# Kernel optimization log

Measured on AMD Instinct MI355X. Metric: run time of the kernel, lower is better.

Reference implementation:

```python
import jax, jax.numpy as jnp
import numpy as np

H = 8              # n_heads
N_PER_GRAPH = 64   # nodes per graph (equal-sized graphs)


def setup_inputs() -> dict:
    key = jax.random.key(0)
    ks = jax.random.split(key, 5)
    total, D = 65536, 512
    x = jax.random.normal(ks[0], (total, D), dtype=jnp.float32)
    batch = jnp.arange(total, dtype=jnp.int64) // N_PER_GRAPH  # sorted graph ids
    s = 1.0 / np.sqrt(D).astype(np.float32)
    # nn.MultiheadAttention packed in-proj (xavier-ish uniform) + zero bias
    in_proj_w = jax.random.uniform(ks[1], (3 * D, D), jnp.float32, -s, s)
    in_proj_b = jnp.zeros((3 * D,), jnp.float32)
    out_proj_w = jax.random.uniform(ks[2], (D, D), jnp.float32, -s, s)
    out_proj_b = jnp.zeros((D,), jnp.float32)
    gate_w = jax.random.uniform(ks[3], (1, D), jnp.float32, -s, s)
    gate_b = jnp.zeros((1,), jnp.float32)
    return {"x": x, "batch": batch, "in_proj_w": in_proj_w, "in_proj_b": in_proj_b,
            "out_proj_w": out_proj_w, "out_proj_b": out_proj_b,
            "gate_w": gate_w, "gate_b": gate_b}


def reference(x, batch, in_proj_w, in_proj_b, out_proj_w, out_proj_b, gate_w, gate_b):
    total, D = x.shape
    G = total // N_PER_GRAPH
    hd = D // H
    xg = x.reshape(G, N_PER_GRAPH, D)                       # [G, N, D]
    # packed qkv projection (torch: x @ in_proj_w.T + in_proj_b)
    qkv = jnp.einsum('gnd,ed->gne', xg, in_proj_w) + in_proj_b
    q, k, v = jnp.split(qkv, 3, axis=-1)
    def to_heads(t):
        return t.reshape(G, N_PER_GRAPH, H, hd).transpose(0, 2, 1, 3)  # [G, H, N, hd]
    q, k, v = to_heads(q), to_heads(k), to_heads(v)
    scores = jnp.einsum('ghnd,ghmd->ghnm', q, k) * (1.0 / np.sqrt(hd))
    attn = jax.nn.softmax(scores, axis=-1)
    ctx = jnp.einsum('ghnm,ghmd->ghnd', attn, v)
    ctx = ctx.transpose(0, 2, 1, 3).reshape(G, N_PER_GRAPH, D)
    attn_out = jnp.einsum('gnd,ed->gne', ctx, out_proj_w) + out_proj_b  # [G, N, D]
    gates = jax.nn.sigmoid(jnp.einsum('gnd,od->gno', attn_out, gate_w) + gate_b)
    return (attn_out * gates).sum(axis=1)                   # [G, D]
```

## Files before the change

### kernel.cpp

```cpp
#include <hip/hip_runtime.h>
#include <stdint.h>


typedef __attribute__((ext_vector_type(8))) short short8;
typedef __attribute__((ext_vector_type(4))) float f32x4;

#define D_ 512

#define WQKV_OFF   0u
#define WO_OFF     1572864u
#define UPART_OFF  2097152u
#define U_OFF      2129920u
#define C0_OFF     2131968u
#define SG_OFF     2132032u
#define WCTX_OFF   2136128u

__device__ __forceinline__ unsigned short f2bf(float f) {
    union { float f; unsigned int u; } t; t.f = f;
    unsigned int u = t.u;
    return (unsigned short)((u + 0x7FFFu + ((u >> 16) & 1u)) >> 16);
}

__global__ __launch_bounds__(256)
void convert_weights(const float* __restrict__ wqkv, const float* __restrict__ wo,
                     unsigned short* __restrict__ wbf) {
    const int i4 = blockIdx.x * 256 + threadIdx.x;
    float4 v;
    if (i4 < 196608) v = *(const float4*)(wqkv + (size_t)i4 * 4);
    else             v = *(const float4*)(wo   + (size_t)(i4 - 196608) * 4);
    unsigned short a0 = f2bf(v.x), a1 = f2bf(v.y), a2 = f2bf(v.z), a3 = f2bf(v.w);
    uint2 p; p.x = a0 | ((unsigned)a1 << 16); p.y = a2 | ((unsigned)a3 << 16);
    *(uint2*)(wbf + (size_t)i4 * 4) = p;
}

__global__ __launch_bounds__(256)
void compute_u_partial(const float* __restrict__ wo, const float* __restrict__ gw,
                       float* __restrict__ upart) {
    const int b = blockIdx.x;
    const int t = threadIdx.x;
    float a0 = 0.f, a1 = 0.f;
    #pragma unroll 4
    for (int e = b * 32; e < b * 32 + 32; ++e) {
        const float ge = gw[e];
        a0 += wo[(size_t)e * 512 + t]       * ge;
        a1 += wo[(size_t)e * 512 + t + 256] * ge;
    }
    upart[b * 512 + t] = a0; upart[b * 512 + t + 256] = a1;
}

__global__ __launch_bounds__(256)
void finalize_u(const float* __restrict__ upart, const float* __restrict__ bo,
                const float* __restrict__ gw, const float* __restrict__ gb,
                float* __restrict__ u, float* __restrict__ c0) {
    const int t = threadIdx.x;
    float s0 = 0.f, s1 = 0.f;
    #pragma unroll
    for (int b = 0; b < 16; ++b) { s0 += upart[b*512 + t]; s1 += upart[b*512 + t + 256]; }
    u[t] = s0; u[t + 256] = s1;
    __shared__ float rb[256];
    rb[t] = bo[t] * gw[t] + bo[t + 256] * gw[t + 256];
    __syncthreads();
    for (int s = 128; s > 0; s >>= 1) { if (t < s) rb[t] += rb[t + s]; __syncthreads(); }
    if (t == 0) c0[0] = rb[0] + gb[0];
}

__global__ __launch_bounds__(512, 2)
void attn_ctx_kernel(const float* __restrict__ x,
                     const unsigned short* __restrict__ wqkv,
                     const float* __restrict__ bqkv,
                     const float* __restrict__ u,
                     const float* __restrict__ c0,
                     unsigned short* __restrict__ wctx_ws,
                     float* __restrict__ sumgate)
{
    __shared__ unsigned short xs[64][520];
    __shared__ unsigned short qbuf[2][64][72];
    __shared__ unsigned short kbuf[2][64][72];
    __shared__ unsigned short vbuf[2][64][72];
    __shared__ unsigned short pbuf[2][64][72];
    __shared__ float fbuf[4][512];
    __shared__ float logit2[2][64];
    __shared__ float gatev[64];

    const int g    = blockIdx.x;
    const int tid  = threadIdx.x;
    const int w    = tid >> 6;
    const int lane = tid & 63;
    const int l15  = lane & 15;
    const int quad = lane >> 4;

    #pragma unroll
    for (int i = 0; i < 16; ++i) {
        int idx = tid + i * 512;
        int row = idx >> 7;
        int c4  = idx & 127;
        float4 v = *(const float4*)(x + ((size_t)(g*64 + row))*512 + c4*4);
        unsigned short a0 = f2bf(v.x), a1 = f2bf(v.y), a2 = f2bf(v.z), a3 = f2bf(v.w);
        uint2 p; p.x = a0 | ((unsigned)a1 << 16); p.y = a2 | ((unsigned)a3 << 16);
        *(uint2*)(&xs[row][c4*4]) = p;
    }
    if (tid < 128) ((float*)logit2)[tid] = 0.f;

    const int hs2  = w >> 2;
    const int row0 = (w & 3) << 4;
    f32x4 cctx[4][4];

    int mj[3], hsj[3], rtj[3];
    #pragma unroll
    for (int j = 0; j < 3; ++j) {
        int t_ = w*3 + j;
        int c  = t_ >> 2; rtj[j] = t_ & 3;
        mj[j]  = c >> 1;  hsj[j] = c & 1;
    }

    #pragma unroll
    for (int hp = 0; hp < 4; ++hp) {
        __syncthreads();

        f32x4 acc[3][4];
        #pragma unroll
        for (int j = 0; j < 3; ++j)
            #pragma unroll
            for (int nt = 0; nt < 4; ++nt) acc[j][nt] = (f32x4){0.f,0.f,0.f,0.f};

        const unsigned short* wr[3];
        #pragma unroll
        for (int j = 0; j < 3; ++j) {
            int head = hp*2 + hsj[j];
            wr[j] = wqkv + (size_t)(mj[j]*512 + head*64 + rtj[j]*16 + l15) * 512;
        }
        #pragma unroll 4
        for (int ks = 0; ks < 16; ++ks) {
            const int col = ks*32 + quad*8;
            short8 a0 = *(const short8*)(wr[0] + col);
            short8 a1 = *(const short8*)(wr[1] + col);
            short8 a2 = *(const short8*)(wr[2] + col);
            #pragma unroll
            for (int nt = 0; nt < 4; ++nt) {
                short8 b = *(const short8*)(&xs[nt*16 + l15][col]);
                acc[0][nt] = __builtin_amdgcn_mfma_f32_16x16x32_bf16(a0, b, acc[0][nt], 0,0,0);
                acc[1][nt] = __builtin_amdgcn_mfma_f32_16x16x32_bf16(a1, b, acc[1][nt], 0,0,0);
                acc[2][nt] = __builtin_amdgcn_mfma_f32_16x16x32_bf16(a2, b, acc[2][nt], 0,0,0);
            }
        }
        #pragma unroll
        for (int j = 0; j < 3; ++j) {
            const int head  = hp*2 + hsj[j];
            const int dbase = mj[j]*512 + head*64 + rtj[j]*16 + quad*4;
            if (mj[j] == 2) {
                #pragma unroll
                for (int nt = 0; nt < 4; ++nt)
                    #pragma unroll
                    for (int r = 0; r < 4; ++r)
                        vbuf[hsj[j]][rtj[j]*16 + quad*4 + r][nt*16 + l15] =
                            f2bf(acc[j][nt][r] + bqkv[dbase + r]);
            } else {
                unsigned short (*dst)[72] = (mj[j] == 0) ? qbuf[hsj[j]] : kbuf[hsj[j]];
                #pragma unroll
                for (int nt = 0; nt < 4; ++nt) {
                    unsigned short tv[4];
                    #pragma unroll
                    for (int r = 0; r < 4; ++r) tv[r] = f2bf(acc[j][nt][r] + bqkv[dbase + r]);
                    uint2 pk; pk.x = tv[0] | ((unsigned)tv[1] << 16);
                    pk.y = tv[2] | ((unsigned)tv[3] << 16);
                    *(uint2*)(&dst[nt*16 + l15][rtj[j]*16 + quad*4]) = pk;
                }
            }
        }
        __syncthreads();

        f32x4 sacc[4];
        #pragma unroll
        for (int i = 0; i < 4; ++i) sacc[i] = (f32x4){0.f,0.f,0.f,0.f};
        #pragma unroll
        for (int ks = 0; ks < 2; ++ks) {
            short8 aq = *(const short8*)(&qbuf[hs2][row0 + l15][ks*32 + quad*8]);
            #pragma unroll
            for (int mt = 0; mt < 4; ++mt) {
                short8 bk = *(const short8*)(&kbuf[hs2][mt*16 + l15][ks*32 + quad*8]);
                sacc[mt] = __builtin_amdgcn_mfma_f32_16x16x32_bf16(aq, bk, sacc[mt], 0,0,0);
            }
        }
        float pv[4][4];
        #pragma unroll
        for (int r = 0; r < 4; ++r) {
            float m0 = -1e30f;
            #pragma unroll
            for (int mt = 0; mt < 4; ++mt) { pv[mt][r] = sacc[mt][r] * 0.125f; m0 = fmaxf(m0, pv[mt][r]); }
            m0 = fmaxf(m0, __shfl_xor(m0, 1));
            m0 = fmaxf(m0, __shfl_xor(m0, 2));
            m0 = fmaxf(m0, __shfl_xor(m0, 4));
            m0 = fmaxf(m0, __shfl_xor(m0, 8));
            float s = 0.f;
            #pragma unroll
            for (int mt = 0; mt < 4; ++mt) { float e = __expf(pv[mt][r] - m0); pv[mt][r] = e; s += e; }
            s += __shfl_xor(s, 1); s += __shfl_xor(s, 2); s += __shfl_xor(s, 4); s += __shfl_xor(s, 8);
            float inv = 1.0f / s;
            #pragma unroll
            for (int mt = 0; mt < 4; ++mt) pv[mt][r] *= inv;
        }
        #pragma unroll
        for (int mt = 0; mt < 4; ++mt)
            #pragma unroll
            for (int r = 0; r < 4; ++r)
                pbuf[hs2][row0 + quad*4 + r][mt*16 + l15] = f2bf(pv[mt][r]);
        __syncthreads();

        #pragma unroll
        for (int i = 0; i < 4; ++i) cctx[hp][i] = (f32x4){0.f,0.f,0.f,0.f};
        #pragma unroll
        for (int ks = 0; ks < 2; ++ks) {
            short8 ap = *(const short8*)(&pbuf[hs2][row0 + l15][ks*32 + quad*8]);
            #pragma unroll
            for (int dt = 0; dt < 4; ++dt) {
                short8 bv = *(const short8*)(&vbuf[hs2][dt*16 + l15][ks*32 + quad*8]);
                cctx[hp][dt] = __builtin_amdgcn_mfma_f32_16x16x32_bf16(ap, bv, cctx[hp][dt], 0,0,0);
            }
        }
        {
            const int head2 = hp*2 + hs2;
            float uv[4];
            #pragma unroll
            for (int dt = 0; dt < 4; ++dt) uv[dt] = u[head2*64 + dt*16 + l15];
            #pragma unroll
            for (int r = 0; r < 4; ++r) {
                float s = cctx[hp][0][r]*uv[0] + cctx[hp][1][r]*uv[1]
                        + cctx[hp][2][r]*uv[2] + cctx[hp][3][r]*uv[3];
                s += __shfl_xor(s, 1); s += __shfl_xor(s, 2);
                s += __shfl_xor(s, 4); s += __shfl_xor(s, 8);
                if (l15 == 0) logit2[hs2][row0 + quad*4 + r] += s;
            }
        }
    }

    __syncthreads();
    if (tid < 64) {
        float lg = logit2[0][tid] + logit2[1][tid] + c0[0];
        float gt = 1.0f / (1.0f + __expf(-lg));
        gatev[tid] = gt;
        float s = gt;
        s += __shfl_xor(s, 1);  s += __shfl_xor(s, 2);  s += __shfl_xor(s, 4);
        s += __shfl_xor(s, 8);  s += __shfl_xor(s, 16); s += __shfl_xor(s, 32);
        if (tid == 0) sumgate[g] = s;
    }
    __syncthreads();

    {
        float gv[4];
        #pragma unroll
        for (int r = 0; r < 4; ++r) gv[r] = gatev[row0 + quad*4 + r];
        #pragma unroll
        for (int hp = 0; hp < 4; ++hp) {
            const int head2 = hp*2 + hs2;
            #pragma unroll
            for (int dt = 0; dt < 4; ++dt) {
                float s = cctx[hp][dt][0]*gv[0] + cctx[hp][dt][1]*gv[1]
                        + cctx[hp][dt][2]*gv[2] + cctx[hp][dt][3]*gv[3];
                s += __shfl_xor(s, 16); s += __shfl_xor(s, 32);
                if (lane < 16) fbuf[w & 3][head2*64 + dt*16 + lane] = s;
            }
        }
    }
    __syncthreads();
    {
        float vs = fbuf[0][tid] + fbuf[1][tid] + fbuf[2][tid] + fbuf[3][tid];
        wctx_ws[(size_t)g*512 + tid] = f2bf(vs);
    }
}

__global__ __launch_bounds__(256, 4)
void outproj_kernel(const unsigned short* __restrict__ wo_bf,
                    const unsigned short* __restrict__ wctx_bf,
                    const float* __restrict__ bo,
                    const float* __restrict__ sumgate,
                    float* __restrict__ out)
{
    const int tid  = threadIdx.x;
    const int w    = tid >> 6;
    const int lane = tid & 63;
    const int l15  = lane & 15;
    const int quad = lane >> 4;
    const int g0   = blockIdx.x * 32;

    f32x4 oac[8][2];
    #pragma unroll
    for (int et = 0; et < 8; ++et)
        #pragma unroll
        for (int mt = 0; mt < 2; ++mt)
            oac[et][mt] = (f32x4){0.f,0.f,0.f,0.f};

    #pragma unroll 4
    for (int ks = 0; ks < 16; ++ks) {
        const int col = ks*32 + quad*8;
        short8 a0 = *(const short8*)(wctx_bf + (size_t)(g0 + l15)*D_      + col);
        short8 a1 = *(const short8*)(wctx_bf + (size_t)(g0 + 16 + l15)*D_ + col);
        #pragma unroll
        for (int et = 0; et < 8; ++et) {
            short8 b = *(const short8*)(wo_bf + (size_t)(w*128 + et*16 + l15)*D_ + col);
            oac[et][0] = __builtin_amdgcn_mfma_f32_16x16x32_bf16(a0, b, oac[et][0], 0,0,0);
            oac[et][1] = __builtin_amdgcn_mfma_f32_16x16x32_bf16(a1, b, oac[et][1], 0,0,0);
        }
    }
    #pragma unroll
    for (int et = 0; et < 8; ++et) {
        const int e = w*128 + et*16 + l15;
        const float bov = bo[e];
        #pragma unroll
        for (int mt = 0; mt < 2; ++mt)
            #pragma unroll
            for (int r = 0; r < 4; ++r) {
                const int gg = g0 + mt*16 + quad*4 + r;
                out[(size_t)gg*D_ + e] = oac[et][mt][r] + sumgate[gg] * bov;
            }
    }
}

extern "C" void kernel_launch(void* const* d_in, const int* in_sizes, int n_in,
                              void* d_out, int out_size, void* d_ws, size_t ws_size,
                              hipStream_t stream) {
    const float* x    = (const float*)d_in[0];
    const float* wqkv = (const float*)d_in[2];
    const float* bqkv = (const float*)d_in[3];
    const float* wo   = (const float*)d_in[4];
    const float* bo   = (const float*)d_in[5];
    const float* gw   = (const float*)d_in[6];
    const float* gb   = (const float*)d_in[7];
    float* out = (float*)d_out;

    char* ws = (char*)d_ws;
    unsigned short* wqkv_bf = (unsigned short*)(ws + WQKV_OFF);
    unsigned short* wo_bf   = (unsigned short*)(ws + WO_OFF);
    float*          upart   = (float*)(ws + UPART_OFF);
    float*          u_ws    = (float*)(ws + U_OFF);
    float*          c0_ws   = (float*)(ws + C0_OFF);
    float*          sg_ws   = (float*)(ws + SG_OFF);
    unsigned short* wctx_ws = (unsigned short*)(ws + WCTX_OFF);

    const int total = in_sizes[0] / D_;
    const int G     = total / 64;

    hipLaunchKernelGGL(convert_weights,   dim3(1024), dim3(256), 0, stream, wqkv, wo, wqkv_bf);
    hipLaunchKernelGGL(compute_u_partial, dim3(16),   dim3(256), 0, stream, wo, gw, upart);
    hipLaunchKernelGGL(finalize_u,        dim3(1),    dim3(256), 0, stream, upart, bo, gw, gb, u_ws, c0_ws);
    hipLaunchKernelGGL(attn_ctx_kernel,   dim3(G),    dim3(512), 0, stream,
                       x, wqkv_bf, bqkv, u_ws, c0_ws, wctx_ws, sg_ws);
    hipLaunchKernelGGL(outproj_kernel,    dim3(G/32), dim3(256), 0, stream,
                       wo_bf, wctx_ws, bo, sg_ws, out);
}
```

Before: 477.5 us.

## Assign one head per wave and keep Q/K in registers to drop block barriers

Each of the 8 waves now owns one attention head end to end: it computes Q, K and V for that head, rearranges Q and K into MFMA operand layout in registers with lane shuffles, and runs scores, softmax and P·V inside the wave. A private per-wave shared-memory scratch holds only V and P. This removes the four head-pair iterations and their repeated __syncthreads. The gated context reduction is also written directly from registers, dropping the fbuf stage. In exchange, register pressure rises (16 score tiles and 16 context tiles per wave), which could cause spills at the 512×2 launch bound. Each wave also issues weight loads for three matrices per d-tile.

```diff
diff --git a/kernel.cpp b/kernel.cpp
--- a/kernel.cpp
+++ b/kernel.cpp
@@ -20,6 +20,9 @@
     unsigned int u = t.u;
     return (unsigned short)((u + 0x7FFFu + ((u >> 16) & 1u)) >> 16);
 }
+__device__ __forceinline__ unsigned pack2(float a, float b) {
+    return (unsigned)f2bf(a) | ((unsigned)f2bf(b) << 16);
+}
 
 __global__ __launch_bounds__(256)
 void convert_weights(const float* __restrict__ wqkv, const float* __restrict__ wo,
@@ -28,8 +31,7 @@
     float4 v;
     if (i4 < 196608) v = *(const float4*)(wqkv + (size_t)i4 * 4);
     else             v = *(const float4*)(wo   + (size_t)(i4 - 196608) * 4);
-    unsigned short a0 = f2bf(v.x), a1 = f2bf(v.y), a2 = f2bf(v.z), a3 = f2bf(v.w);
-    uint2 p; p.x = a0 | ((unsigned)a1 << 16); p.y = a2 | ((unsigned)a3 << 16);
+    uint2 p; p.x = pack2(v.x, v.y); p.y = pack2(v.z, v.w);
     *(uint2*)(wbf + (size_t)i4 * 4) = p;
 }
 
@@ -64,6 +66,8 @@
     if (t == 0) c0[0] = rb[0] + gb[0];
 }
 
+union U8 { unsigned u[4]; short8 s; };
+
 __global__ __launch_bounds__(512, 2)
 void attn_ctx_kernel(const float* __restrict__ x,
                      const unsigned short* __restrict__ wqkv,
@@ -74,12 +78,8 @@
                      float* __restrict__ sumgate)
 {
     __shared__ unsigned short xs[64][520];
-    __shared__ unsigned short qbuf[2][64][72];
-    __shared__ unsigned short kbuf[2][64][72];
-    __shared__ unsigned short vbuf[2][64][72];
-    __shared__ unsigned short pbuf[2][64][72];
-    __shared__ float fbuf[4][512];
-    __shared__ float logit2[2][64];
+    __shared__ unsigned short scr[8][64][72];
+    __shared__ float logitp[8][64];
     __shared__ float gatev[64];
 
     const int g    = blockIdx.x;
@@ -95,147 +95,165 @@
         int row = idx >> 7;
         int c4  = idx & 127;
         float4 v = *(const float4*)(x + ((size_t)(g*64 + row))*512 + c4*4);
-        unsigned short a0 = f2bf(v.x), a1 = f2bf(v.y), a2 = f2bf(v.z), a3 = f2bf(v.w);
-        uint2 p; p.x = a0 | ((unsigned)a1 << 16); p.y = a2 | ((unsigned)a3 << 16);
+        uint2 p; p.x = pack2(v.x, v.y); p.y = pack2(v.z, v.w);
         *(uint2*)(&xs[row][c4*4]) = p;
     }
-    if (tid < 128) ((float*)logit2)[tid] = 0.f;
-
-    const int hs2  = w >> 2;
-    const int row0 = (w & 3) << 4;
-    f32x4 cctx[4][4];
-
-    int mj[3], hsj[3], rtj[3];
-    #pragma unroll
-    for (int j = 0; j < 3; ++j) {
-        int t_ = w*3 + j;
-        int c  = t_ >> 2; rtj[j] = t_ & 3;
-        mj[j]  = c >> 1;  hsj[j] = c & 1;
-    }
-
-    #pragma unroll
-    for (int hp = 0; hp < 4; ++hp) {
-        __syncthreads();
-
-        f32x4 acc[3][4];
-        #pragma unroll
-        for (int j = 0; j < 3; ++j)
-            #pragma unroll
-            for (int nt = 0; nt < 4; ++nt) acc[j][nt] = (f32x4){0.f,0.f,0.f,0.f};
-
-        const unsigned short* wr[3];
-        #pragma unroll
-        for (int j = 0; j < 3; ++j) {
-            int head = hp*2 + hsj[j];
-            wr[j] = wqkv + (size_t)(mj[j]*512 + head*64 + rtj[j]*16 + l15) * 512;
-        }
+    __syncthreads();
+
+    const int h = w;
+    unsigned short (*S)[72] = scr[w];
+
+    U8 qA[4][2], kB[4][2];
+    #pragma unroll
+    for (int dt = 0; dt < 4; ++dt) {
+        f32x4 aq[4], ak[4], av[4];
+        #pragma unroll
+        for (int nt = 0; nt < 4; ++nt) {
+            aq[nt] = (f32x4){0.f,0.f,0.f,0.f};
+            ak[nt] = (f32x4){0.f,0.f,0.f,0.f};
+            av[nt] = (f32x4){0.f,0.f,0.f,0.f};
+        }
+        const unsigned short* wq = wqkv + (size_t)(          h*64 + dt*16 + l15) * 512;
+        const unsigned short* wk = wqkv + (size_t)( 512 +    h*64 + dt*16 + l15) * 512;
+        const unsigned short* wv = wqkv + (size_t)(1024 +    h*64 + dt*16 + l15) * 512;
         #pragma unroll 4
         for (int ks = 0; ks < 16; ++ks) {
             const int col = ks*32 + quad*8;
-            short8 a0 = *(const short8*)(wr[0] + col);
-            short8 a1 = *(const short8*)(wr[1] + col);
-            short8 a2 = *(const short8*)(wr[2] + col);
+            short8 a0 = *(const short8*)(wq + col);
+            short8 a1 = *(const short8*)(wk + col);
+            short8 a2 = *(const short8*)(wv + col);
             #pragma unroll
             for (int nt = 0; nt < 4; ++nt) {
                 short8 b = *(const short8*)(&xs[nt*16 + l15][col]);
-                acc[0][nt] = __builtin_amdgcn_mfma_f32_16x16x32_bf16(a0, b, acc[0][nt], 0,0,0);
-                acc[1][nt] = __builtin_amdgcn_mfma_f32_16x16x32_bf16(a1, b, acc[1][nt], 0,0,0);
-                acc[2][nt] = __builtin_amdgcn_mfma_f32_16x16x32_bf16(a2, b, acc[2][nt], 0,0,0);
-            }
-        }
-        #pragma unroll
-        for (int j = 0; j < 3; ++j) {
-            const int head  = hp*2 + hsj[j];
-            const int dbase = mj[j]*512 + head*64 + rtj[j]*16 + quad*4;
-            if (mj[j] == 2) {
-                #pragma unroll
-                for (int nt = 0; nt < 4; ++nt)
-                    #pragma unroll
-                    for (int r = 0; r < 4; ++r)
-                        vbuf[hsj[j]][rtj[j]*16 + quad*4 + r][nt*16 + l15] =
-                            f2bf(acc[j][nt][r] + bqkv[dbase + r]);
-            } else {
-                unsigned short (*dst)[72] = (mj[j] == 0) ? qbuf[hsj[j]] : kbuf[hsj[j]];
-                #pragma unroll
-                for (int nt = 0; nt < 4; ++nt) {
-                    unsigned short tv[4];
-                    #pragma unroll
-                    for (int r = 0; r < 4; ++r) tv[r] = f2bf(acc[j][nt][r] + bqkv[dbase + r]);
-                    uint2 pk; pk.x = tv[0] | ((unsigned)tv[1] << 16);
-                    pk.y = tv[2] | ((unsigned)tv[3] << 16);
-                    *(uint2*)(&dst[nt*16 + l15][rtj[j]*16 + quad*4]) = pk;
-                }
-            }
-        }
-        __syncthreads();
-
-        f32x4 sacc[4];
-        #pragma unroll
-        for (int i = 0; i < 4; ++i) sacc[i] = (f32x4){0.f,0.f,0.f,0.f};
-        #pragma unroll
-        for (int ks = 0; ks < 2; ++ks) {
-            short8 aq = *(const short8*)(&qbuf[hs2][row0 + l15][ks*32 + quad*8]);
-            #pragma unroll
-            for (int mt = 0; mt < 4; ++mt) {
-                short8 bk = *(const short8*)(&kbuf[hs2][mt*16 + l15][ks*32 + quad*8]);
-                sacc[mt] = __builtin_amdgcn_mfma_f32_16x16x32_bf16(aq, bk, sacc[mt], 0,0,0);
-            }
-        }
-        float pv[4][4];
+                aq[nt] = __builtin_amdgcn_mfma_f32_16x16x32_bf16(a0, b, aq[nt], 0,0,0);
+                ak[nt] = __builtin_amdgcn_mfma_f32_16x16x32_bf16(a1, b, ak[nt], 0,0,0);
+                av[nt] = __builtin_amdgcn_mfma_f32_16x16x32_bf16(a2, b, av[nt], 0,0,0);
+            }
+        }
+        float bq[4], bk2[4], bv2[4];
+        #pragma unroll
+        for (int r = 0; r < 4; ++r) {
+            bq[r]  = bqkv[          h*64 + dt*16 + quad*4 + r];
+            bk2[r] = bqkv[ 512 +    h*64 + dt*16 + quad*4 + r];
+            bv2[r] = bqkv[1024 +    h*64 + dt*16 + quad*4 + r];
+        }
+        const bool take = ((quad >> 1) == (dt & 1));
+        const int  ks2  = dt >> 1;
+        #pragma unroll
+        for (int nt = 0; nt < 4; ++nt) {
+            unsigned q01 = pack2(aq[nt][0]+bq[0],  aq[nt][1]+bq[1]);
+            unsigned q23 = pack2(aq[nt][2]+bq[2],  aq[nt][3]+bq[3]);
+            unsigned k01 = pack2(ak[nt][0]+bk2[0], ak[nt][1]+bk2[1]);
+            unsigned k23 = pack2(ak[nt][2]+bk2[2], ak[nt][3]+bk2[3]);
+            #pragma unroll
+            for (int j = 0; j < 4; ++j) {
+                int srcl = ((quad & 1)*2 + (j >> 1))*16 + l15;
+                unsigned tq = (unsigned)__shfl((int)((j & 1) ? q23 : q01), srcl);
+                unsigned tk = (unsigned)__shfl((int)((j & 1) ? k23 : k01), srcl);
+                if (take) { qA[nt][ks2].u[j] = tq; kB[nt][ks2].u[j] = tk; }
+            }
+            #pragma unroll
+            for (int r = 0; r < 4; ++r)
+                S[dt*16 + quad*4 + r][nt*16 + l15] = f2bf(av[nt][r] + bv2[r]);
+        }
+    }
+
+    f32x4 sacc[4][4];
+    #pragma unroll
+    for (int a = 0; a < 4; ++a)
+        #pragma unroll
+        for (int b = 0; b < 4; ++b) sacc[a][b] = (f32x4){0.f,0.f,0.f,0.f};
+    #pragma unroll
+    for (int ks2 = 0; ks2 < 2; ++ks2)
+        #pragma unroll
+        for (int a = 0; a < 4; ++a)
+            #pragma unroll
+            for (int b = 0; b < 4; ++b)
+                sacc[a][b] = __builtin_amdgcn_mfma_f32_16x16x32_bf16(
+                                 qA[a][ks2].s, kB[b][ks2].s, sacc[a][b], 0,0,0);
+
+    #pragma unroll
+    for (int a = 0; a < 4; ++a) {
         #pragma unroll
         for (int r = 0; r < 4; ++r) {
             float m0 = -1e30f;
             #pragma unroll
-            for (int mt = 0; mt < 4; ++mt) { pv[mt][r] = sacc[mt][r] * 0.125f; m0 = fmaxf(m0, pv[mt][r]); }
+            for (int b = 0; b < 4; ++b) { sacc[a][b][r] *= 0.125f; m0 = fmaxf(m0, sacc[a][b][r]); }
             m0 = fmaxf(m0, __shfl_xor(m0, 1));
             m0 = fmaxf(m0, __shfl_xor(m0, 2));
             m0 = fmaxf(m0, __shfl_xor(m0, 4));
             m0 = fmaxf(m0, __shfl_xor(m0, 8));
             float s = 0.f;
             #pragma unroll
-            for (int mt = 0; mt < 4; ++mt) { float e = __expf(pv[mt][r] - m0); pv[mt][r] = e; s += e; }
+            for (int b = 0; b < 4; ++b) { float e = __expf(sacc[a][b][r] - m0); sacc[a][b][r] = e; s += e; }
             s += __shfl_xor(s, 1); s += __shfl_xor(s, 2); s += __shfl_xor(s, 4); s += __shfl_xor(s, 8);
             float inv = 1.0f / s;
             #pragma unroll
-            for (int mt = 0; mt < 4; ++mt) pv[mt][r] *= inv;
-        }
-        #pragma unroll
-        for (int mt = 0; mt < 4; ++mt)
+            for (int b = 0; b < 4; ++b) sacc[a][b][r] *= inv;
+        }
+    }
+
+    U8 vA[4][2];
+    #pragma unroll
+    for (int dtile = 0; dtile < 4; ++dtile)
+        #pragma unroll
+        for (int ks2 = 0; ks2 < 2; ++ks2)
+            vA[dtile][ks2].s = *(const short8*)(&S[dtile*16 + l15][ks2*32 + quad*8]);
+
+    #pragma unroll
+    for (int a = 0; a < 4; ++a)
+        #pragma unroll
+        for (int b = 0; b < 4; ++b)
             #pragma unroll
             for (int r = 0; r < 4; ++r)
-                pbuf[hs2][row0 + quad*4 + r][mt*16 + l15] = f2bf(pv[mt][r]);
-        __syncthreads();
-
-        #pragma unroll
-        for (int i = 0; i < 4; ++i) cctx[hp][i] = (f32x4){0.f,0.f,0.f,0.f};
-        #pragma unroll
-        for (int ks = 0; ks < 2; ++ks) {
-            short8 ap = *(const short8*)(&pbuf[hs2][row0 + l15][ks*32 + quad*8]);
-            #pragma unroll
-            for (int dt = 0; dt < 4; ++dt) {
-                short8 bv = *(const short8*)(&vbuf[hs2][dt*16 + l15][ks*32 + quad*8]);
-                cctx[hp][dt] = __builtin_amdgcn_mfma_f32_16x16x32_bf16(ap, bv, cctx[hp][dt], 0,0,0);
-            }
-        }
-        {
-            const int head2 = hp*2 + hs2;
-            float uv[4];
-            #pragma unroll
-            for (int dt = 0; dt < 4; ++dt) uv[dt] = u[head2*64 + dt*16 + l15];
-            #pragma unroll
-            for (int r = 0; r < 4; ++r) {
-                float s = cctx[hp][0][r]*uv[0] + cctx[hp][1][r]*uv[1]
-                        + cctx[hp][2][r]*uv[2] + cctx[hp][3][r]*uv[3];
-                s += __shfl_xor(s, 1); s += __shfl_xor(s, 2);
-                s += __shfl_xor(s, 4); s += __shfl_xor(s, 8);
-                if (l15 == 0) logit2[hs2][row0 + quad*4 + r] += s;
-            }
-        }
-    }
-
+                S[a*16 + quad*4 + r][b*16 + l15] = f2bf(sacc[a][b][r]);
+
+    U8 pB[4][2];
+    #pragma unroll
+    for (int a = 0; a < 4; ++a)
+        #pragma unroll
+        for (int ks2 = 0; ks2 < 2; ++ks2)
+            pB[a][ks2].s = *(const short8*)(&S[a*16 + l15][ks2*32 + quad*8]);
+
+    f32x4 cacc[4][4];
+    #pragma unroll
+    for (int dtile = 0; dtile < 4; ++dtile)
+        #pragma unroll
+        for (int a = 0; a < 4; ++a) cacc[dtile][a] = (f32x4){0.f,0.f,0.f,0.f};
+    #pragma unroll
+    for (int ks2 = 0; ks2 < 2; ++ks2)
+        #pragma unroll
+        for (int dtile = 0; dtile < 4; ++dtile)
+            #pragma unroll
+            for (int a = 0; a < 4; ++a)
+                cacc[dtile][a] = __builtin_amdgcn_mfma_f32_16x16x32_bf16(
+                                     vA[dtile][ks2].s, pB[a][ks2].s, cacc[dtile][a], 0,0,0);
+
+    {
+        float uv[4][4];
+        #pragma unroll
+        for (int dtile = 0; dtile < 4; ++dtile)
+            #pragma unroll
+            for (int r = 0; r < 4; ++r)
+                uv[dtile][r] = u[h*64 + dtile*16 + quad*4 + r];
+        #pragma unroll
+        for (int a = 0; a < 4; ++a) {
+            float s = 0.f;
+            #pragma unroll
+            for (int dtile = 0; dtile < 4; ++dtile)
+                #pragma unroll
+                for (int r = 0; r < 4; ++r)
+                    s += cacc[dtile][a][r] * uv[dtile][r];
+            s += __shfl_xor(s, 16); s += __shfl_xor(s, 32);
+            if (quad == 0) logitp[w][a*16 + l15] = s;
+        }
+    }
     __syncthreads();
+
     if (tid < 64) {
-        float lg = logit2[0][tid] + logit2[1][tid] + c0[0];
+        float lg = c0[0];
+        #pragma unroll
+        for (int ww = 0; ww < 8; ++ww) lg += logitp[ww][tid];
         float gt = 1.0f / (1.0f + __expf(-lg));
         gatev[tid] = gt;
         float s = gt;
@@ -248,23 +266,23 @@
     {
         float gv[4];
         #pragma unroll
-        for (int r = 0; r < 4; ++r) gv[r] = gatev[row0 + quad*4 + r];
-        #pragma unroll
-        for (int hp = 0; hp < 4; ++hp) {
-            const int head2 = hp*2 + hs2;
-            #pragma unroll
-            for (int dt = 0; dt < 4; ++dt) {
-                float s = cctx[hp][dt][0]*gv[0] + cctx[hp][dt][1]*gv[1]
-                        + cctx[hp][dt][2]*gv[2] + cctx[hp][dt][3]*gv[3];
-                s += __shfl_xor(s, 16); s += __shfl_xor(s, 32);
-                if (lane < 16) fbuf[w & 3][head2*64 + dt*16 + lane] = s;
-            }
-        }
-    }
-    __syncthreads();
-    {
-        float vs = fbuf[0][tid] + fbuf[1][tid] + fbuf[2][tid] + fbuf[3][tid];
-        wctx_ws[(size_t)g*512 + tid] = f2bf(vs);
+        for (int a = 0; a < 4; ++a) gv[a] = gatev[a*16 + l15];
+        #pragma unroll
+        for (int dtile = 0; dtile < 4; ++dtile) {
+            float sr[4];
+            #pragma unroll
+            for (int r = 0; r < 4; ++r) {
+                float s = cacc[dtile][0][r]*gv[0] + cacc[dtile][1][r]*gv[1]
+                        + cacc[dtile][2][r]*gv[2] + cacc[dtile][3][r]*gv[3];
+                s += __shfl_xor(s, 1); s += __shfl_xor(s, 2);
+                s += __shfl_xor(s, 4); s += __shfl_xor(s, 8);
+                sr[r] = s;
+            }
+            if (l15 == 0) {
+                uint2 pk; pk.x = pack2(sr[0], sr[1]); pk.y = pack2(sr[2], sr[3]);
+                *(uint2*)(wctx_ws + (size_t)g*512 + h*64 + dtile*16 + quad*4) = pk;
+            }
+        }
     }
 }
 
```

New measurement: 445.8 us. 1.07x faster.
